# Kernel optimization log

Hardware: AMD Instinct MI355X
Metric: run time of the kernel (lower is better)

Reference implementation:

```python
import jax, jax.numpy as jnp
import numpy as np

NEG_INF = -1e9


def setup_inputs() -> dict:
    key = jax.random.key(0)
    ks = jax.random.split(key, 9)
    B, T, E, D, H = 64, 2048, 1024, 1024, 1024
    enc = jax.random.normal(ks[0], (B, T, E), dtype=jnp.float32)
    dec = jax.random.normal(ks[1], (B, D), dtype=jnp.float32)
    inp_mask = jax.random.randint(ks[2], (B, T), 0, 2, dtype=jnp.int32)
    s = 1.0 / np.sqrt(H)
    W_enc = jax.random.normal(ks[3], (E, H), dtype=jnp.float32) * s
    b_enc = jax.random.normal(ks[4], (H,), dtype=jnp.float32) * 0.01
    W_dec = jax.random.normal(ks[5], (D, H), dtype=jnp.float32) * s
    b_dec = jax.random.normal(ks[6], (H,), dtype=jnp.float32) * 0.01
    W_out = jax.random.normal(ks[7], (H, 1), dtype=jnp.float32) * s
    b_out = jax.random.normal(ks[8], (1,), dtype=jnp.float32) * 0.01
    return {"enc": enc, "dec": dec, "inp_mask": inp_mask,
            "W_enc": W_enc, "b_enc": b_enc, "W_dec": W_dec, "b_dec": b_dec,
            "W_out": W_out, "b_out": b_out}


def reference(enc, dec, inp_mask, W_enc, b_enc, W_dec, b_dec, W_out, b_out):
    # a: [B, T, H] = Linear(enc) + Linear(dec)[:, None, :]
    a = jnp.einsum('bte,eh->bth', enc, W_enc) + b_enc \
        + (dec @ W_dec + b_dec)[:, None, :]
    a = jnp.tanh(a)
    # scores: [B, T]
    scores = (jnp.einsum('bth,h->bt', a, W_out[:, 0]) + b_out[0])
    scores = jnp.where(inp_mask == 0, NEG_INF, scores)
    probs = jax.nn.softmax(scores, axis=1)            # [B, T]
    attn = jnp.einsum('bt,bte->be', probs, enc)       # [B, E]
    return (attn, probs)
```

## Files before the change

kernel.cpp:

```cpp
#include <hip/hip_runtime.h>
#include <hip/hip_bf16.h>

typedef __attribute__((ext_vector_type(4))) float f32x4;
typedef __attribute__((ext_vector_type(4))) unsigned int u32x4;
typedef __attribute__((ext_vector_type(8))) short s16x8;

static constexpr int Bb = 64;
static constexpr int Tt = 2048;
static constexpr int Ee = 1024;
static constexpr int Hh = 1024;
static constexpr int ATTN_N = Bb * Ee;
static constexpr int PROB_N = Bb * Tt;

__device__ inline unsigned short f2bf(float f) {
    __hip_bfloat16 h = __float2bfloat16(f);
    return __builtin_bit_cast(unsigned short, h);
}

__device__ inline void gload_lds16(const unsigned short* g, unsigned short* l) {
    __builtin_amdgcn_global_load_lds(
        (const __attribute__((address_space(1))) void*)g,
        (__attribute__((address_space(3))) void*)l,
        16, 0, 0);
}

__global__ void wtrans_kernel(const float* __restrict__ w_enc,
                              unsigned short* __restrict__ w16t) {
    __shared__ float tile[32][33];
    const int bx = blockIdx.x & 31;
    const int by = blockIdx.x >> 5;
    const int tx = threadIdx.x & 31;
    const int ty = threadIdx.x >> 5;
#pragma unroll
    for (int j = 0; j < 4; ++j) {
        int e = by * 32 + ty + j * 8;
        int h = bx * 32 + tx;
        tile[ty + j * 8][tx] = w_enc[e * Hh + h];
    }
    __syncthreads();
#pragma unroll
    for (int j = 0; j < 4; ++j) {
        int h = bx * 32 + ty + j * 8;
        int e = by * 32 + tx;
        w16t[h * Ee + e] = f2bf(tile[tx][ty + j * 8]);
    }
}

__global__ void ddec_kernel(const float* __restrict__ dec,
                            const float* __restrict__ w_dec,
                            const float* __restrict__ b_dec,
                            const float* __restrict__ b_enc,
                            float* __restrict__ ddec) {
    const int b = blockIdx.y;
    const int h = blockIdx.x * 256 + threadIdx.x;
    float acc = b_dec[h] + b_enc[h];
    const float* dr = dec + b * Ee;
#pragma unroll 4
    for (int e = 0; e < Ee; ++e) {
        acc += dr[e] * w_dec[e * Hh + h];
    }
    ddec[b * Hh + h] = acc;
}

__global__ __launch_bounds__(512, 1) void gemm_score_kernel(
    const float* __restrict__ enc, const unsigned short* __restrict__ w16t,
    const float* __restrict__ ddec, const float* __restrict__ w_out,
    float* __restrict__ scores) {
    __shared__ unsigned short As[2][256 * 64];
    __shared__ unsigned short Bs[2][256 * 64];

    const int tid = threadIdx.x;
    const int lane = tid & 63;
    const int wid = tid >> 6;
    const int wm = wid >> 2;
    const int wn = wid & 3;
    const int lr = lane & 15;
    const int lg = lane >> 4;

    const int g = blockIdx.x;
    const int xcd = g & 7;
    const int slot = g >> 3;
    const int ntile = slot & 3;
    const int mtile = xcd * 64 + (slot >> 2);
    const int m0 = mtile * 256;
    const int n0 = ntile * 256;
    const int bidx = m0 >> 11;

    const int ar = tid >> 3;
    const int as = tid & 7;

    f32x4 rs[8];

    auto loadA = [&](int kt) {
        const float* src = enc + (size_t)(m0 + ar) * Ee + kt * 64 + as * 8;
#pragma unroll
        for (int ci = 0; ci < 4; ++ci) {
            rs[ci * 2]     = *reinterpret_cast<const f32x4*>(src + (size_t)(64 * ci) * Ee);
            rs[ci * 2 + 1] = *reinterpret_cast<const f32x4*>(src + (size_t)(64 * ci) * Ee + 4);
        }
    };
    auto writeA = [&](int db) {
        char* abase = (char*)&As[db][0];
#pragma unroll
        for (int ci = 0; ci < 4; ++ci) {
            int r = ar + 64 * ci;
            u32x4 w;
            w.x = (unsigned)f2bf(rs[2 * ci].x) | ((unsigned)f2bf(rs[2 * ci].y) << 16);
            w.y = (unsigned)f2bf(rs[2 * ci].z) | ((unsigned)f2bf(rs[2 * ci].w) << 16);
            w.z = (unsigned)f2bf(rs[2 * ci + 1].x) | ((unsigned)f2bf(rs[2 * ci + 1].y) << 16);
            w.w = (unsigned)f2bf(rs[2 * ci + 1].z) | ((unsigned)f2bf(rs[2 * ci + 1].w) << 16);
            *reinterpret_cast<u32x4*>(abase + r * 128 + ((as * 16) ^ ((r & 7) << 4))) = w;
        }
    };
    auto stageB = [&](int kt, int db) {
        const int sg = (lane & 7) ^ (lane >> 3);
#pragma unroll
        for (int c = 0; c < 4; ++c) {
            int rr = (wid * 4 + c) * 8 + (lane >> 3);
            const unsigned short* src = w16t + (size_t)(n0 + rr) * Ee + kt * 64 + sg * 8;
            gload_lds16(src, &Bs[db][(wid * 4 + c) * 512]);
        }
    };

    f32x4 acc[8][4];
#pragma unroll
    for (int ni = 0; ni < 4; ++ni) {
        float dv = ddec[bidx * Hh + n0 + wn * 64 + ni * 16 + lr];
#pragma unroll
        for (int mi = 0; mi < 8; ++mi) {
            acc[mi][ni].x = dv; acc[mi][ni].y = dv;
            acc[mi][ni].z = dv; acc[mi][ni].w = dv;
        }
    }

    u32x4 af[4], bf[4];
    auto readB4 = [&](int db, int kh) {
        const char* bbase = (const char*)&Bs[db][0];
        const int kb = kh * 64 + lg * 16;
#pragma unroll
        for (int ni = 0; ni < 4; ++ni) {
            int r = wn * 64 + ni * 16 + lr;
            bf[ni] = *reinterpret_cast<const u32x4*>(bbase + r * 128 + (kb ^ ((r & 7) << 4)));
        }
    };
    auto readA4 = [&](int db, int kh, int mib) {
        const char* abase = (const char*)&As[db][0];
        const int kb = kh * 64 + lg * 16;
#pragma unroll
        for (int k = 0; k < 4; ++k) {
            int r = wm * 128 + (mib + k) * 16 + lr;
            af[k] = *reinterpret_cast<const u32x4*>(abase + r * 128 + (kb ^ ((r & 7) << 4)));
        }
    };
    auto mfma16 = [&](int mib) {
        __builtin_amdgcn_s_setprio(1);
#pragma unroll
        for (int k = 0; k < 4; ++k)
#pragma unroll
            for (int ni = 0; ni < 4; ++ni)
                acc[mib + k][ni] = __builtin_amdgcn_mfma_f32_16x16x32_bf16(
                    __builtin_bit_cast(s16x8, af[k]),
                    __builtin_bit_cast(s16x8, bf[ni]),
                    acc[mib + k][ni], 0, 0, 0);
        __builtin_amdgcn_s_setprio(0);
    };

#define BARRIER() do { asm volatile("" ::: "memory"); \
    __builtin_amdgcn_s_barrier(); asm volatile("" ::: "memory"); } while (0)
#define LGKM0() asm volatile("s_waitcnt lgkmcnt(0)" ::: "memory")

    loadA(0);
    writeA(0);
    LGKM0();
    stageB(0, 0);
    loadA(1);
    asm volatile("s_waitcnt vmcnt(8)" ::: "memory");
    BARRIER();

#pragma unroll 1
    for (int t = 0; t < 16; ++t) {
        const int p = t & 1;
        readB4(p, 0);
        readA4(p, 0, 0);
        if (t < 15) stageB(t + 1, p ^ 1);
        BARRIER(); LGKM0();
        mfma16(0);
        BARRIER();
        readA4(p, 0, 4);
        BARRIER(); LGKM0();
        mfma16(4);
        BARRIER();
        readB4(p, 1);
        readA4(p, 1, 0);
        BARRIER(); LGKM0();
        mfma16(0);
        BARRIER();
        readA4(p, 1, 4);
        if (t < 15) writeA(p ^ 1);
        BARRIER(); LGKM0();
        if (t < 14) {
            loadA(t + 2);
            asm volatile("s_waitcnt vmcnt(8)" ::: "memory");
        } else if (t == 14) {
            asm volatile("s_waitcnt vmcnt(0)" ::: "memory");
        }
        mfma16(4);
        BARRIER();
    }

    float wout[4];
#pragma unroll
    for (int ni = 0; ni < 4; ++ni)
        wout[ni] = w_out[n0 + wn * 64 + ni * 16 + lr];

#pragma unroll
    for (int mi = 0; mi < 8; ++mi) {
#pragma unroll
        for (int i = 0; i < 4; ++i) {
            float s = 0.f;
#pragma unroll
            for (int ni = 0; ni < 4; ++ni) {
                float x = (i == 0) ? acc[mi][ni].x : (i == 1) ? acc[mi][ni].y
                           : (i == 2) ? acc[mi][ni].z : acc[mi][ni].w;
                float t = 1.f - 2.f / (__expf(2.f * x) + 1.f);
                s += t * wout[ni];
            }
            s += __shfl_xor(s, 1);
            s += __shfl_xor(s, 2);
            s += __shfl_xor(s, 4);
            s += __shfl_xor(s, 8);
            if (lr == 0) {
                int row = m0 + wm * 128 + mi * 16 + 4 * lg + i;
                atomicAdd(&scores[row], s);
            }
        }
    }
#undef BARRIER
#undef LGKM0
}

__global__ __launch_bounds__(256) void softmax_kernel(float* __restrict__ sc,
                                                      const int* __restrict__ mask) {
    __shared__ float red[256];
    const int b = blockIdx.x;
    const int tid = threadIdx.x;
    float* row = sc + b * Tt;
    const int* mrow = mask + b * Tt;

    float v[8];
    float mx = -3.0e38f;
#pragma unroll
    for (int j = 0; j < 8; ++j) {
        int t = tid + j * 256;
        float s = row[t];
        v[j] = (mrow[t] == 0) ? -1.0e9f : s;
        mx = fmaxf(mx, v[j]);
    }
    red[tid] = mx;
    __syncthreads();
    for (int off = 128; off > 0; off >>= 1) {
        if (tid < off) red[tid] = fmaxf(red[tid], red[tid + off]);
        __syncthreads();
    }
    mx = red[0];
    __syncthreads();

    float p[8];
    float sum = 0.f;
#pragma unroll
    for (int j = 0; j < 8; ++j) {
        p[j] = __expf(v[j] - mx);
        sum += p[j];
    }
    red[tid] = sum;
    __syncthreads();
    for (int off = 128; off > 0; off >>= 1) {
        if (tid < off) red[tid] += red[tid + off];
        __syncthreads();
    }
    float inv = 1.f / red[0];
#pragma unroll
    for (int j = 0; j < 8; ++j)
        row[tid + j * 256] = p[j] * inv;
}

__global__ __launch_bounds__(256) void attn_kernel(const float* __restrict__ enc,
                                                   const float* __restrict__ probs,
                                                   float* __restrict__ attn) {
    __shared__ float pr[128];
    const int b = blockIdx.y;
    const int tc = blockIdx.x;
    const int tid = threadIdx.x;
    if (tid < 128) pr[tid] = probs[b * Tt + tc * 128 + tid];
    __syncthreads();

    const int e0 = tid * 4;
    f32x4 acc; acc.x = 0.f; acc.y = 0.f; acc.z = 0.f; acc.w = 0.f;
    const float* base = enc + (size_t)b * Tt * Ee + (size_t)tc * 128 * Ee + e0;
#pragma unroll 4
    for (int t = 0; t < 128; ++t) {
        f32x4 vv = *reinterpret_cast<const f32x4*>(base + (size_t)t * Ee);
        float pw = pr[t];
        acc.x += pw * vv.x; acc.y += pw * vv.y;
        acc.z += pw * vv.z; acc.w += pw * vv.w;
    }
    atomicAdd(&attn[b * Ee + e0 + 0], acc.x);
    atomicAdd(&attn[b * Ee + e0 + 1], acc.y);
    atomicAdd(&attn[b * Ee + e0 + 2], acc.z);
    atomicAdd(&attn[b * Ee + e0 + 3], acc.w);
}

extern "C" void kernel_launch(void* const* d_in, const int* in_sizes, int n_in,
                              void* d_out, int out_size, void* d_ws, size_t ws_size,
                              hipStream_t stream) {
    const float* enc      = (const float*)d_in[0];
    const float* dec      = (const float*)d_in[1];
    const int*   inp_mask = (const int*)d_in[2];
    const float* W_enc    = (const float*)d_in[3];
    const float* b_enc    = (const float*)d_in[4];
    const float* W_dec    = (const float*)d_in[5];
    const float* b_dec    = (const float*)d_in[6];
    const float* W_out    = (const float*)d_in[7];

    float* attn   = (float*)d_out;
    float* scores = (float*)d_out + ATTN_N;

    unsigned short* w16t = (unsigned short*)d_ws;
    float* ddec = attn;

    hipMemsetAsync(scores, 0, (size_t)PROB_N * sizeof(float), stream);

    wtrans_kernel<<<dim3(1024), 256, 0, stream>>>(W_enc, w16t);
    ddec_kernel<<<dim3(4, 64), 256, 0, stream>>>(dec, W_dec, b_dec, b_enc, ddec);
    gemm_score_kernel<<<dim3(2048), 512, 0, stream>>>(enc, w16t, ddec, W_out, scores);

    hipMemsetAsync(attn, 0, (size_t)ATTN_N * sizeof(float), stream);

    softmax_kernel<<<dim3(64), 256, 0, stream>>>(scores, inp_mask);
    attn_kernel<<<dim3(16, 64), 256, 0, stream>>>(enc, scores, attn);
}
```

Measured before the change: 642.3 us.

## Pre-convert enc to bf16 in workspace for async-LDS GEMM and attention

Adds a pass that converts the full fp32 encoder tensor to bf16 in workspace. A new GEMM kernel then streams bf16 A tiles straight into LDS with global_load_lds, instead of loading fp32 and converting in registers. The attention-weighted sum also reads the bf16 copy, halving its bytes. The price is an extra full read of the fp32 tensor plus a bf16 write, a large workspace requirement (the old path is kept as a fallback when workspace is too small), and bf16 rounding of enc in the attention output.

```diff
diff --git a/kernel.cpp b/kernel.cpp
--- a/kernel.cpp
+++ b/kernel.cpp
@@ -3,6 +3,7 @@
 
 typedef __attribute__((ext_vector_type(4))) float f32x4;
 typedef __attribute__((ext_vector_type(4))) unsigned int u32x4;
+typedef __attribute__((ext_vector_type(2))) unsigned int u32x2;
 typedef __attribute__((ext_vector_type(8))) short s16x8;
 
 static constexpr int Bb = 64;
@@ -15,6 +16,9 @@
 __device__ inline unsigned short f2bf(float f) {
     __hip_bfloat16 h = __float2bfloat16(f);
     return __builtin_bit_cast(unsigned short, h);
+}
+__device__ inline float bf2f(unsigned short u) {
+    return __builtin_bit_cast(float, (unsigned)u << 16);
 }
 
 __device__ inline void gload_lds16(const unsigned short* g, unsigned short* l) {
@@ -60,6 +64,176 @@
         acc += dr[e] * w_dec[e * Hh + h];
     }
     ddec[b * Hh + h] = acc;
+}
+
+__global__ __launch_bounds__(256) void e2bf_kernel(const float* __restrict__ src,
+                                                   unsigned short* __restrict__ dst,
+                                                   long long n8) {
+    long long i = (long long)blockIdx.x * 256 + threadIdx.x;
+    const long long stride = (long long)gridDim.x * 256;
+    for (; i < n8; i += stride) {
+        const f32x4* s = reinterpret_cast<const f32x4*>(src + i * 8);
+        f32x4 a = s[0], b = s[1];
+        u32x4 w;
+        w.x = (unsigned)f2bf(a.x) | ((unsigned)f2bf(a.y) << 16);
+        w.y = (unsigned)f2bf(a.z) | ((unsigned)f2bf(a.w) << 16);
+        w.z = (unsigned)f2bf(b.x) | ((unsigned)f2bf(b.y) << 16);
+        w.w = (unsigned)f2bf(b.z) | ((unsigned)f2bf(b.w) << 16);
+        *reinterpret_cast<u32x4*>(dst + i * 8) = w;
+    }
+}
+
+__global__ __launch_bounds__(512, 1) void gemm_score_bf16a(
+    const unsigned short* __restrict__ a16, const unsigned short* __restrict__ w16t,
+    const float* __restrict__ ddec, const float* __restrict__ w_out,
+    float* __restrict__ scores) {
+    __shared__ unsigned short As[2][256 * 64];
+    __shared__ unsigned short Bs[2][256 * 64];
+
+    const int tid = threadIdx.x;
+    const int lane = tid & 63;
+    const int wid = tid >> 6;
+    const int wm = wid >> 2;
+    const int wn = wid & 3;
+    const int lr = lane & 15;
+    const int lg = lane >> 4;
+
+    const int g = blockIdx.x;
+    const int xcd = g & 7;
+    const int slot = g >> 3;
+    const int ntile = slot & 3;
+    const int mtile = xcd * 64 + (slot >> 2);
+    const int m0 = mtile * 256;
+    const int n0 = ntile * 256;
+    const int bidx = m0 >> 11;
+
+    const int sg = (lane & 7) ^ (lane >> 3);
+    auto stageA = [&](int kt, int db) {
+#pragma unroll
+        for (int c = 0; c < 4; ++c) {
+            int rr = (wid * 4 + c) * 8 + (lane >> 3);
+            const unsigned short* src = a16 + (size_t)(m0 + rr) * Ee + kt * 64 + sg * 8;
+            gload_lds16(src, &As[db][(wid * 4 + c) * 512]);
+        }
+    };
+    auto stageB = [&](int kt, int db) {
+#pragma unroll
+        for (int c = 0; c < 4; ++c) {
+            int rr = (wid * 4 + c) * 8 + (lane >> 3);
+            const unsigned short* src = w16t + (size_t)(n0 + rr) * Ee + kt * 64 + sg * 8;
+            gload_lds16(src, &Bs[db][(wid * 4 + c) * 512]);
+        }
+    };
+
+    f32x4 acc[8][4];
+#pragma unroll
+    for (int ni = 0; ni < 4; ++ni) {
+        float dv = ddec[bidx * Hh + n0 + wn * 64 + ni * 16 + lr];
+#pragma unroll
+        for (int mi = 0; mi < 8; ++mi) {
+            acc[mi][ni].x = dv; acc[mi][ni].y = dv;
+            acc[mi][ni].z = dv; acc[mi][ni].w = dv;
+        }
+    }
+
+    u32x4 af[4], bf[4];
+    auto readB4 = [&](int db, int kh) {
+        const char* bbase = (const char*)&Bs[db][0];
+        const int kb = kh * 64 + lg * 16;
+#pragma unroll
+        for (int ni = 0; ni < 4; ++ni) {
+            int r = wn * 64 + ni * 16 + lr;
+            bf[ni] = *reinterpret_cast<const u32x4*>(bbase + r * 128 + (kb ^ ((r & 7) << 4)));
+        }
+    };
+    auto readA4 = [&](int db, int kh, int mib) {
+        const char* abase = (const char*)&As[db][0];
+        const int kb = kh * 64 + lg * 16;
+#pragma unroll
+        for (int k = 0; k < 4; ++k) {
+            int r = wm * 128 + (mib + k) * 16 + lr;
+            af[k] = *reinterpret_cast<const u32x4*>(abase + r * 128 + (kb ^ ((r & 7) << 4)));
+        }
+    };
+    auto mfma16 = [&](int mib) {
+        __builtin_amdgcn_s_setprio(1);
+#pragma unroll
+        for (int k = 0; k < 4; ++k)
+#pragma unroll
+            for (int ni = 0; ni < 4; ++ni)
+                acc[mib + k][ni] = __builtin_amdgcn_mfma_f32_16x16x32_bf16(
+                    __builtin_bit_cast(s16x8, af[k]),
+                    __builtin_bit_cast(s16x8, bf[ni]),
+                    acc[mib + k][ni], 0, 0, 0);
+        __builtin_amdgcn_s_setprio(0);
+    };
+
+#define BARRIER() do { asm volatile("" ::: "memory"); \
+    __builtin_amdgcn_s_barrier(); asm volatile("" ::: "memory"); } while (0)
+#define LGKM0() asm volatile("s_waitcnt lgkmcnt(0)" ::: "memory")
+
+    stageA(0, 0);
+    stageB(0, 0);
+    asm volatile("s_waitcnt vmcnt(0)" ::: "memory");
+    BARRIER();
+
+#pragma unroll 1
+    for (int tt = 0; tt < 16; tt += 2) {
+#pragma unroll
+        for (int p = 0; p < 2; ++p) {
+            const int t = tt + p;
+            readB4(p, 0);
+            readA4(p, 0, 0);
+            if (t < 15) { stageA(t + 1, p ^ 1); stageB(t + 1, p ^ 1); }
+            BARRIER(); LGKM0();
+            mfma16(0);
+            BARRIER();
+            readA4(p, 0, 4);
+            BARRIER(); LGKM0();
+            mfma16(4);
+            BARRIER();
+            readB4(p, 1);
+            readA4(p, 1, 0);
+            BARRIER(); LGKM0();
+            mfma16(0);
+            BARRIER();
+            readA4(p, 1, 4);
+            if (t < 15) asm volatile("s_waitcnt vmcnt(0)" ::: "memory");
+            BARRIER(); LGKM0();
+            mfma16(4);
+            BARRIER();
+        }
+    }
+
+    float wout[4];
+#pragma unroll
+    for (int ni = 0; ni < 4; ++ni)
+        wout[ni] = w_out[n0 + wn * 64 + ni * 16 + lr];
+
+#pragma unroll
+    for (int mi = 0; mi < 8; ++mi) {
+#pragma unroll
+        for (int i = 0; i < 4; ++i) {
+            float s = 0.f;
+#pragma unroll
+            for (int ni = 0; ni < 4; ++ni) {
+                float x = (i == 0) ? acc[mi][ni].x : (i == 1) ? acc[mi][ni].y
+                           : (i == 2) ? acc[mi][ni].z : acc[mi][ni].w;
+                float t = 1.f - 2.f / (__expf(2.f * x) + 1.f);
+                s += t * wout[ni];
+            }
+            s += __shfl_xor(s, 1);
+            s += __shfl_xor(s, 2);
+            s += __shfl_xor(s, 4);
+            s += __shfl_xor(s, 8);
+            if (lr == 0) {
+                int row = m0 + wm * 128 + mi * 16 + 4 * lg + i;
+                atomicAdd(&scores[row], s);
+            }
+        }
+    }
+#undef BARRIER
+#undef LGKM0
 }
 
 __global__ __launch_bounds__(512, 1) void gemm_score_kernel(
@@ -310,6 +484,34 @@
     atomicAdd(&attn[b * Ee + e0 + 3], acc.w);
 }
 
+__global__ __launch_bounds__(256) void attn_kernel_bf16(
+    const unsigned short* __restrict__ enc16,
+    const float* __restrict__ probs, float* __restrict__ attn) {
+    __shared__ float pr[128];
+    const int b = blockIdx.y;
+    const int tc = blockIdx.x;
+    const int tid = threadIdx.x;
+    if (tid < 128) pr[tid] = probs[b * Tt + tc * 128 + tid];
+    __syncthreads();
+
+    const int e0 = tid * 4;
+    f32x4 acc; acc.x = 0.f; acc.y = 0.f; acc.z = 0.f; acc.w = 0.f;
+    const unsigned short* base = enc16 + (size_t)b * Tt * Ee + (size_t)tc * 128 * Ee + e0;
+#pragma unroll 4
+    for (int t = 0; t < 128; ++t) {
+        u32x2 w = *reinterpret_cast<const u32x2*>(base + (size_t)t * Ee);
+        float pw = pr[t];
+        acc.x += pw * bf2f((unsigned short)(w.x & 0xffff));
+        acc.y += pw * bf2f((unsigned short)(w.x >> 16));
+        acc.z += pw * bf2f((unsigned short)(w.y & 0xffff));
+        acc.w += pw * bf2f((unsigned short)(w.y >> 16));
+    }
+    atomicAdd(&attn[b * Ee + e0 + 0], acc.x);
+    atomicAdd(&attn[b * Ee + e0 + 1], acc.y);
+    atomicAdd(&attn[b * Ee + e0 + 2], acc.z);
+    atomicAdd(&attn[b * Ee + e0 + 3], acc.w);
+}
+
 extern "C" void kernel_launch(void* const* d_in, const int* in_sizes, int n_in,
                               void* d_out, int out_size, void* d_ws, size_t ws_size,
                               hipStream_t stream) {
@@ -326,16 +528,34 @@
     float* scores = (float*)d_out + ATTN_N;
 
     unsigned short* w16t = (unsigned short*)d_ws;
+    const size_t W16T_BYTES = (size_t)Hh * Ee * 2;
+    const size_t ENC16_BYTES = (size_t)Bb * Tt * Ee * 2;
+    const bool fast = ws_size >= W16T_BYTES + ENC16_BYTES;
+    unsigned short* enc16 = (unsigned short*)((char*)d_ws + W16T_BYTES);
+
     float* ddec = attn;
 
     hipMemsetAsync(scores, 0, (size_t)PROB_N * sizeof(float), stream);
 
     wtrans_kernel<<<dim3(1024), 256, 0, stream>>>(W_enc, w16t);
     ddec_kernel<<<dim3(4, 64), 256, 0, stream>>>(dec, W_dec, b_dec, b_enc, ddec);
-    gemm_score_kernel<<<dim3(2048), 512, 0, stream>>>(enc, w16t, ddec, W_out, scores);
+
+    if (fast) {
+        e2bf_kernel<<<dim3(2048), 256, 0, stream>>>(
+            enc, enc16, (long long)Bb * Tt * Ee / 8);
+        gemm_score_bf16a<<<dim3(2048), 512, 0, stream>>>(
+            enc16, w16t, ddec, W_out, scores);
+    } else {
+        gemm_score_kernel<<<dim3(2048), 512, 0, stream>>>(
+            enc, w16t, ddec, W_out, scores);
+    }
 
     hipMemsetAsync(attn, 0, (size_t)ATTN_N * sizeof(float), stream);
 
     softmax_kernel<<<dim3(64), 256, 0, stream>>>(scores, inp_mask);
-    attn_kernel<<<dim3(16, 64), 256, 0, stream>>>(enc, scores, attn);
-}
+    if (fast) {
+        attn_kernel_bf16<<<dim3(16, 64), 256, 0, stream>>>(enc16, scores, attn);
+    } else {
+        attn_kernel<<<dim3(16, 64), 256, 0, stream>>>(enc, scores, attn);
+    }
+}
```

Result: slower. 735.4 us (+14.5%).

## Emit bf16 copy of enc from GEMM and use it in attention pass

Applied to the files above, without the earlier changes.

GEMM blocks with ntile 0 now store the bf16-converted A tile they already build to a workspace buffer. A new attention kernel then reads this bf16 copy instead of the fp32 encoder tensor, halving the bytes it reads. The trade is an extra 256MB write inside the GEMM and lower precision in the attention sum. The path is taken only when the workspace is large enough; otherwise the original fp32 kernel runs.

```diff
diff --git a/kernel.cpp b/kernel.cpp
--- a/kernel.cpp
+++ b/kernel.cpp
@@ -3,6 +3,7 @@
 
 typedef __attribute__((ext_vector_type(4))) float f32x4;
 typedef __attribute__((ext_vector_type(4))) unsigned int u32x4;
+typedef __attribute__((ext_vector_type(2))) unsigned int u32x2;
 typedef __attribute__((ext_vector_type(8))) short s16x8;
 
 static constexpr int Bb = 64;
@@ -15,6 +16,9 @@
 __device__ inline unsigned short f2bf(float f) {
     __hip_bfloat16 h = __float2bfloat16(f);
     return __builtin_bit_cast(unsigned short, h);
+}
+__device__ inline float bf2f(unsigned short u) {
+    return __builtin_bit_cast(float, (unsigned)u << 16);
 }
 
 __device__ inline void gload_lds16(const unsigned short* g, unsigned short* l) {
@@ -65,7 +69,8 @@
 __global__ __launch_bounds__(512, 1) void gemm_score_kernel(
     const float* __restrict__ enc, const unsigned short* __restrict__ w16t,
     const float* __restrict__ ddec, const float* __restrict__ w_out,
-    float* __restrict__ scores) {
+    float* __restrict__ scores, unsigned short* __restrict__ enc16out,
+    int doWrite16) {
     __shared__ unsigned short As[2][256 * 64];
     __shared__ unsigned short Bs[2][256 * 64];
 
@@ -88,6 +93,7 @@
 
     const int ar = tid >> 3;
     const int as = tid & 7;
+    const bool st16 = doWrite16 && (ntile == 0);
 
     f32x4 rs[8];
 
@@ -99,7 +105,7 @@
             rs[ci * 2 + 1] = *reinterpret_cast<const f32x4*>(src + (size_t)(64 * ci) * Ee + 4);
         }
     };
-    auto writeA = [&](int db) {
+    auto writeA = [&](int db, int kt) {
         char* abase = (char*)&As[db][0];
 #pragma unroll
         for (int ci = 0; ci < 4; ++ci) {
@@ -110,6 +116,9 @@
             w.z = (unsigned)f2bf(rs[2 * ci + 1].x) | ((unsigned)f2bf(rs[2 * ci + 1].y) << 16);
             w.w = (unsigned)f2bf(rs[2 * ci + 1].z) | ((unsigned)f2bf(rs[2 * ci + 1].w) << 16);
             *reinterpret_cast<u32x4*>(abase + r * 128 + ((as * 16) ^ ((r & 7) << 4))) = w;
+            if (st16)
+                *reinterpret_cast<u32x4*>(
+                    enc16out + (size_t)(m0 + r) * Ee + kt * 64 + as * 8) = w;
         }
     };
     auto stageB = [&](int kt, int db) {
@@ -170,7 +179,7 @@
 #define LGKM0() asm volatile("s_waitcnt lgkmcnt(0)" ::: "memory")
 
     loadA(0);
-    writeA(0);
+    writeA(0, 0);
     LGKM0();
     stageB(0, 0);
     loadA(1);
@@ -196,7 +205,7 @@
         mfma16(0);
         BARRIER();
         readA4(p, 1, 4);
-        if (t < 15) writeA(p ^ 1);
+        if (t < 15) writeA(p ^ 1, t + 1);
         BARRIER(); LGKM0();
         if (t < 14) {
             loadA(t + 2);
@@ -310,6 +319,34 @@
     atomicAdd(&attn[b * Ee + e0 + 3], acc.w);
 }
 
+__global__ __launch_bounds__(256) void attn_kernel_bf16(
+    const unsigned short* __restrict__ enc16,
+    const float* __restrict__ probs, float* __restrict__ attn) {
+    __shared__ float pr[128];
+    const int b = blockIdx.y;
+    const int tc = blockIdx.x;
+    const int tid = threadIdx.x;
+    if (tid < 128) pr[tid] = probs[b * Tt + tc * 128 + tid];
+    __syncthreads();
+
+    const int e0 = tid * 4;
+    f32x4 acc; acc.x = 0.f; acc.y = 0.f; acc.z = 0.f; acc.w = 0.f;
+    const unsigned short* base = enc16 + (size_t)b * Tt * Ee + (size_t)tc * 128 * Ee + e0;
+#pragma unroll 4
+    for (int t = 0; t < 128; ++t) {
+        u32x2 w = *reinterpret_cast<const u32x2*>(base + (size_t)t * Ee);
+        float pw = pr[t];
+        acc.x += pw * bf2f((unsigned short)(w.x & 0xffff));
+        acc.y += pw * bf2f((unsigned short)(w.x >> 16));
+        acc.z += pw * bf2f((unsigned short)(w.y & 0xffff));
+        acc.w += pw * bf2f((unsigned short)(w.y >> 16));
+    }
+    atomicAdd(&attn[b * Ee + e0 + 0], acc.x);
+    atomicAdd(&attn[b * Ee + e0 + 1], acc.y);
+    atomicAdd(&attn[b * Ee + e0 + 2], acc.z);
+    atomicAdd(&attn[b * Ee + e0 + 3], acc.w);
+}
+
 extern "C" void kernel_launch(void* const* d_in, const int* in_sizes, int n_in,
                               void* d_out, int out_size, void* d_ws, size_t ws_size,
                               hipStream_t stream) {
@@ -326,16 +363,28 @@
     float* scores = (float*)d_out + ATTN_N;
 
     unsigned short* w16t = (unsigned short*)d_ws;
+    const size_t W16T_BYTES = (size_t)Hh * Ee * 2;
+    const size_t ENC16_BYTES = (size_t)Bb * Tt * Ee * 2;
+    const bool fast = ws_size >= W16T_BYTES + ENC16_BYTES;
+    unsigned short* enc16 = (unsigned short*)((char*)d_ws + W16T_BYTES);
+
     float* ddec = attn;
 
     hipMemsetAsync(scores, 0, (size_t)PROB_N * sizeof(float), stream);
 
     wtrans_kernel<<<dim3(1024), 256, 0, stream>>>(W_enc, w16t);
     ddec_kernel<<<dim3(4, 64), 256, 0, stream>>>(dec, W_dec, b_dec, b_enc, ddec);
-    gemm_score_kernel<<<dim3(2048), 512, 0, stream>>>(enc, w16t, ddec, W_out, scores);
+
+    gemm_score_kernel<<<dim3(2048), 512, 0, stream>>>(
+        enc, w16t, ddec, W_out, scores, fast ? enc16 : (unsigned short*)nullptr,
+        fast ? 1 : 0);
 
     hipMemsetAsync(attn, 0, (size_t)ATTN_N * sizeof(float), stream);
 
     softmax_kernel<<<dim3(64), 256, 0, stream>>>(scores, inp_mask);
-    attn_kernel<<<dim3(16, 64), 256, 0, stream>>>(enc, scores, attn);
-}
+    if (fast) {
+        attn_kernel_bf16<<<dim3(16, 64), 256, 0, stream>>>(enc16, scores, attn);
+    } else {
+        attn_kernel<<<dim3(16, 64), 256, 0, stream>>>(enc, scores, attn);
+    }
+}
```

After: 684.8 us. 6.6% more time.

## Drop intra-iteration barriers and unroll GEMM main loop by two

Applied to the files above, without the earlier changes.

Removes the barriers and lgkmcnt waits between each LDS read and MFMA group, leaving a single barrier per K-step. The loop is also unrolled by two so the double-buffer parity is a compile-time constant. The aim is to stop waves serialising on frequent barriers and let the compiler interleave LDS reads with MFMAs. It risks races: writeA into the other buffer now sits mid-iteration with no barrier before the buffer is read, and the compiler memory fences were removed.

```diff
diff --git a/kernel.cpp b/kernel.cpp
--- a/kernel.cpp
+++ b/kernel.cpp
@@ -165,8 +165,6 @@
         __builtin_amdgcn_s_setprio(0);
     };
 
-#define BARRIER() do { asm volatile("" ::: "memory"); \
-    __builtin_amdgcn_s_barrier(); asm volatile("" ::: "memory"); } while (0)
 #define LGKM0() asm volatile("s_waitcnt lgkmcnt(0)" ::: "memory")
 
     loadA(0);
@@ -175,37 +173,28 @@
     stageB(0, 0);
     loadA(1);
     asm volatile("s_waitcnt vmcnt(8)" ::: "memory");
-    BARRIER();
+    __builtin_amdgcn_s_barrier();
 
 #pragma unroll 1
-    for (int t = 0; t < 16; ++t) {
-        const int p = t & 1;
-        readB4(p, 0);
-        readA4(p, 0, 0);
-        if (t < 15) stageB(t + 1, p ^ 1);
-        BARRIER(); LGKM0();
-        mfma16(0);
-        BARRIER();
-        readA4(p, 0, 4);
-        BARRIER(); LGKM0();
-        mfma16(4);
-        BARRIER();
-        readB4(p, 1);
-        readA4(p, 1, 0);
-        BARRIER(); LGKM0();
-        mfma16(0);
-        BARRIER();
-        readA4(p, 1, 4);
-        if (t < 15) writeA(p ^ 1);
-        BARRIER(); LGKM0();
-        if (t < 14) {
-            loadA(t + 2);
-            asm volatile("s_waitcnt vmcnt(8)" ::: "memory");
-        } else if (t == 14) {
-            asm volatile("s_waitcnt vmcnt(0)" ::: "memory");
-        }
-        mfma16(4);
-        BARRIER();
+    for (int tt = 0; tt < 16; tt += 2) {
+#pragma unroll
+        for (int pp = 0; pp < 2; ++pp) {
+            const int t = tt + pp;
+            if (t < 15) stageB(t + 1, pp ^ 1);
+            readB4(pp, 0); readA4(pp, 0, 0); mfma16(0);
+            readA4(pp, 0, 4);                mfma16(4);
+            if (t < 15) writeA(pp ^ 1);
+            readB4(pp, 1); readA4(pp, 1, 0); mfma16(0);
+            readA4(pp, 1, 4);                mfma16(4);
+            LGKM0();
+            if (t < 14) {
+                loadA(t + 2);
+                asm volatile("s_waitcnt vmcnt(8)" ::: "memory");
+            } else if (t == 14) {
+                asm volatile("s_waitcnt vmcnt(0)" ::: "memory");
+            }
+            __builtin_amdgcn_s_barrier();
+        }
     }
 
     float wout[4];
@@ -235,7 +224,6 @@
             }
         }
     }
-#undef BARRIER
 #undef LGKM0
 }
 
```

After: 773.1 us. +20.4%, slower.
